# Kernel tuning notes

Hardware: AMD Instinct MI355X
Metric: run time of the kernel (lower is better)

The kernel has to match this reference:

```python
import jax, jax.numpy as jnp
import numpy as np

NUM_HEADS = 8


def setup_inputs() -> dict:
    key = jax.random.key(0)
    ks = jax.random.split(key, 6)
    B, S, H = 2, 4096, 512
    Q = jax.random.normal(ks[0], (B, S, H), dtype=jnp.float32)
    K = jax.random.normal(ks[1], (B, S, H), dtype=jnp.float32)
    V = jax.random.normal(ks[2], (B, S, H), dtype=jnp.float32)
    risk_sigma = jax.random.uniform(ks[3], (B, 1), dtype=jnp.float32) * 0.2
    risk_lambda = jnp.array([2.0], dtype=jnp.float32)
    W_out = jax.random.normal(ks[4], (H, H), dtype=jnp.float32) * (1.0 / np.sqrt(H))
    b_out = jnp.zeros((H,), dtype=jnp.float32)
    return {"Q": Q, "K": K, "V": V, "risk_sigma": risk_sigma,
            "risk_lambda": risk_lambda, "W_out": W_out, "b_out": b_out}


def reference(Q, K, V, risk_sigma, risk_lambda, W_out, b_out):
    B, S, H = Q.shape
    nh = NUM_HEADS
    hd = H // nh
    # split heads: [B, S, nh, hd]
    q = Q.reshape(B, S, nh, hd)
    k = K.reshape(B, S, nh, hd)
    v = V.reshape(B, S, nh, hd)
    scale = 1.0 / jnp.sqrt(jnp.asarray(hd, dtype=Q.dtype))
    # [B, nh, S, S]
    scores = jnp.einsum('bshd,bthd->bhst', q, k) * scale
    # distance-based risk penalty
    pos = jnp.arange(S, dtype=Q.dtype)
    norm_dist = jnp.abs(pos[None, :] - pos[:, None]) / S  # [S, S]
    dist_sq = norm_dist ** 2
    sigma_c = jnp.clip(risk_sigma, 0.001, 0.2)            # [B, 1]
    sigma_n = (sigma_c - 0.001) / (0.2 - 0.001)
    lam = (risk_lambda / 10.0).reshape(())                 # scalar
    risk_term = lam * sigma_n[:, :, None, None] * dist_sq[None, None]  # [B,1,S,S]
    attn = jax.nn.softmax(scores - risk_term, axis=-1)
    ctx = jnp.einsum('bhst,bthd->bshd', attn, v).reshape(B, S, H)
    return ctx @ W_out.T + b_out
```

## Files before the change

### kernel.cpp

```cpp
#include <hip/hip_runtime.h>
#include <hip/hip_bf16.h>


#define S_LEN 4096
#define NHEAD 8
#define HD 64
#define HTOT 512

typedef __attribute__((ext_vector_type(8))) short short8;
typedef __attribute__((ext_vector_type(4))) float floatx4;

#if __has_builtin(__builtin_amdgcn_exp2f)
#define EXP2F(x) __builtin_amdgcn_exp2f(x)
#else
#define EXP2F(x) exp2f(x)
#endif

__device__ __forceinline__ unsigned pack_bf16(float a, float b) {
    unsigned ua = __builtin_bit_cast(unsigned, a) + 0x8000u;
    unsigned ub = __builtin_bit_cast(unsigned, b) + 0x8000u;
    return __builtin_amdgcn_perm(ub, ua, 0x07060302u);
}

__device__ __forceinline__ unsigned short f2bf(float x) {
    unsigned u = __builtin_bit_cast(unsigned, x) + 0x8000u;
    return (unsigned short)(u >> 16);
}

__device__ __forceinline__ void async16(const unsigned short* g, unsigned short* l) {
    __builtin_amdgcn_global_load_lds(
        (const __attribute__((address_space(1))) unsigned int*)g,
        (__attribute__((address_space(3))) unsigned int*)l, 16, 0, 0);
}

__global__ __launch_bounds__(256) void prep_kernel(
    const float* __restrict__ K, unsigned short* __restrict__ K16,
    const float* __restrict__ V, unsigned short* __restrict__ Vt,
    const float* __restrict__ W, unsigned short* __restrict__ W16)
{
    const int tid = threadIdx.x;
    if (blockIdx.x >= 3072) {
        size_t i = ((size_t)(blockIdx.x - 3072) * 256 + tid) * 8;
        float4 a = *(const float4*)(W + i);
        float4 b = *(const float4*)(W + i + 4);
        unsigned o[4] = {pack_bf16(a.x, a.y), pack_bf16(a.z, a.w),
                         pack_bf16(b.x, b.y), pack_bf16(b.z, b.w)};
        *(short8*)(W16 + i) = *(short8*)o;
    } else if (blockIdx.x < 2048) {
        size_t i = ((size_t)blockIdx.x * 256 + tid) * 8;
        float4 a = *(const float4*)(K + i);
        float4 b = *(const float4*)(K + i + 4);
        unsigned o[4] = {pack_bf16(a.x, a.y), pack_bf16(a.z, a.w),
                         pack_bf16(b.x, b.y), pack_bf16(b.z, b.w)};
        *(short8*)(K16 + i) = *(short8*)o;
    } else {
        __shared__ unsigned short T[64 * 66];
        const int blk = blockIdx.x - 2048;
        const int st = blk & 63;
        const int bh = blk >> 6;
        const int b = bh >> 3, h = bh & 7;
        const float* src = V + ((size_t)b * S_LEN + st * 64) * HTOT + h * HD;
        for (int i = 0; i < 4; i++) {
            int idx = tid + i * 256;
            int s = idx >> 4, c4 = idx & 15;
            float4 v = *(const float4*)(src + (size_t)s * HTOT + c4 * 4);
            T[(c4 * 4 + 0) * 66 + s] = f2bf(v.x);
            T[(c4 * 4 + 1) * 66 + s] = f2bf(v.y);
            T[(c4 * 4 + 2) * 66 + s] = f2bf(v.z);
            T[(c4 * 4 + 3) * 66 + s] = f2bf(v.w);
        }
        __syncthreads();
        unsigned short* dst = Vt + ((size_t)bh * 64) * S_LEN + st * 64;
        for (int i = 0; i < 2; i++) {
            int idx = tid + i * 256;
            int d = idx >> 3, c8 = idx & 7;
            uint2 lo = *(const uint2*)&T[d * 66 + c8 * 8];
            uint2 hi = *(const uint2*)&T[d * 66 + c8 * 8 + 4];
            unsigned o[4] = {lo.x, lo.y, hi.x, hi.y};
            *(short8*)(dst + (size_t)d * S_LEN + c8 * 8) = *(short8*)o;
        }
    }
}

__global__ __launch_bounds__(512, 4) void attn_kernel(
    const float* __restrict__ Q, const unsigned short* __restrict__ K16,
    const unsigned short* __restrict__ Vt,
    const float* __restrict__ risk_sigma, const float* __restrict__ risk_lambda,
    unsigned short* __restrict__ ctx)
{
    __shared__ unsigned short SH[32768];

    const int tid  = threadIdx.x;
    const int wave = tid >> 6;
    const int grp  = wave >> 2;
    const int wv   = wave & 3;
    const int lane = tid & 63;
    const int quad = lane >> 4;
    const int ln   = lane & 15;
    const int sw   = ln & 7;

    const int bid = blockIdx.x;
    const int qt  = bid & 31;
    const int h   = (bid >> 5) & 7;
    const int b   = bid >> 8;
    const int qbase = qt * 128;

    float sig = risk_sigma[b];
    sig = fminf(fmaxf(sig, 0.001f), 0.2f);
    const float sn   = (sig - 0.001f) * (1.0f / 0.199f);
    const float coef = risk_lambda[0] * 0.1f * sn;
    const float nc2 = -coef * (1.0f / 4096.0f) * (1.0f / 4096.0f) * 1.4426950408889634f;
    const float qscale = 0.125f * 1.4426950408889634f;

    const float* Qb = Q + (size_t)b * S_LEN * HTOT + (size_t)h * HD;
    const unsigned short* Kb = K16 + (size_t)b * S_LEN * HTOT + (size_t)h * HD;
    const unsigned short* Vb = Vt + ((size_t)(b * 8 + h) * 64) * S_LEN;

    const int rl  = lane >> 3;
    const int c8g = ((lane & 7) ^ rl) << 3;
    const int ksrow = ((wv & 1) << 4) | (((rl >> 2) & 1) << 3)
                    | ((wv >> 1) << 2) | (rl & 3);

    auto dma = [&](int buf, int kb) {
        unsigned short* base = SH + (grp * 2 + buf) * 8192;
        const unsigned short* gk = Kb + (size_t)(kb + ksrow) * HTOT + c8g;
        const unsigned short* gv = Vb + (size_t)(wv * 8 + rl) * S_LEN + kb + c8g;
        async16(gk,              base + wv * 512 + lane * 8);
        async16(gk + 32 * HTOT,  base + (wv + 4) * 512 + lane * 8);
        async16(gv,              base + 4096 + wv * 512 + lane * 8);
        async16(gv + 32 * S_LEN, base + 4096 + (wv + 4) * 512 + lane * 8);
    };

    const int kb0 = grp * 2048;
    dma(0, kb0);

    short8 qf[2][2];
    {
        const float* qp0 = Qb + (size_t)(qbase + wv * 32 + ln) * HTOT + quad * 8;
        #pragma unroll
        for (int nt = 0; nt < 2; nt++) {
            const float* qp = qp0 + (size_t)(nt * 16) * HTOT;
            #pragma unroll
            for (int half = 0; half < 2; half++) {
                float4 x = *(const float4*)(qp + half * 32);
                float4 y = *(const float4*)(qp + half * 32 + 4);
                unsigned o[4] = {pack_bf16(x.x * qscale, x.y * qscale),
                                 pack_bf16(x.z * qscale, x.w * qscale),
                                 pack_bf16(y.x * qscale, y.y * qscale),
                                 pack_bf16(y.z * qscale, y.w * qscale)};
                qf[nt][half] = *(short8*)o;
            }
        }
    }
    __syncthreads();

    const short sone = (short)0x3F80;
    const short8 ones = {sone, sone, sone, sone, sone, sone, sone, sone};

    floatx4 Oacc[2][4], Lacc[2];
    #pragma unroll
    for (int nt = 0; nt < 2; nt++) {
        Lacc[nt] = (floatx4){0.f, 0.f, 0.f, 0.f};
        #pragma unroll
        for (int dt = 0; dt < 4; dt++) Oacc[nt][dt] = (floatx4){0.f, 0.f, 0.f, 0.f};
    }

    const int qa = qbase + wv * 32;
    const float quad8f = (float)(quad * 8);

    for (int kt = 0; kt < 32; ++kt) {
        const int kbase = kb0 + kt * 64;
        const int cur = kt & 1;
        if (kt < 31) dma(1 - cur, kbase + 64);
        const unsigned short* Kc = SH + (grp * 2 + cur) * 8192;
        const unsigned short* Vc = Kc + 4096;

        const float dqq = (float)(qa + ln - kbase) - quad8f;
        unsigned pw[2][2][4];

        #pragma unroll
        for (int jt = 0; jt < 4; jt++) {
            const int krow = (jt * 16 + ln) * 64;
            short8 ak0 = *(const short8*)&Kc[krow + ((quad ^ sw) << 3)];
            short8 ak1 = *(const short8*)&Kc[krow + (((quad + 4) ^ sw) << 3)];
            const float jtoff = (float)((jt >> 1) * 32 + (jt & 1) * 4);
            #pragma unroll
            for (int nt = 0; nt < 2; nt++) {
                float d = dqq + ((float)(nt * 16) - jtoff);
                floatx4 rk;
                #pragma unroll
                for (int r = 0; r < 4; r++) {
                    rk[r] = (nc2 * d) * d;
                    d -= 1.0f;
                }
                floatx4 s = __builtin_amdgcn_mfma_f32_16x16x32_bf16(ak0, qf[nt][0], rk, 0, 0, 0);
                s = __builtin_amdgcn_mfma_f32_16x16x32_bf16(ak1, qf[nt][1], s, 0, 0, 0);
                float p0 = EXP2F(s[0]);
                float p1 = EXP2F(s[1]);
                float p2 = EXP2F(s[2]);
                float p3 = EXP2F(s[3]);
                pw[nt][jt >> 1][(jt & 1) * 2 + 0] = pack_bf16(p0, p1);
                pw[nt][jt >> 1][(jt & 1) * 2 + 1] = pack_bf16(p2, p3);
            }
        }

        __builtin_amdgcn_s_setprio(1);
        #pragma unroll
        for (int dt = 0; dt < 4; dt++) {
            const int vrow = (dt * 16 + ln) * 64;
            short8 bv0 = *(const short8*)&Vc[vrow + ((quad ^ sw) << 3)];
            short8 bv1 = *(const short8*)&Vc[vrow + (((quad + 4) ^ sw) << 3)];
            #pragma unroll
            for (int nt = 0; nt < 2; nt++) {
                short8 pa0 = *(const short8*)&pw[nt][0][0];
                short8 pa1 = *(const short8*)&pw[nt][1][0];
                Oacc[nt][dt] = __builtin_amdgcn_mfma_f32_16x16x32_bf16(pa0, bv0, Oacc[nt][dt], 0, 0, 0);
                Oacc[nt][dt] = __builtin_amdgcn_mfma_f32_16x16x32_bf16(pa1, bv1, Oacc[nt][dt], 0, 0, 0);
            }
        }
        #pragma unroll
        for (int nt = 0; nt < 2; nt++) {
            short8 pa0 = *(const short8*)&pw[nt][0][0];
            short8 pa1 = *(const short8*)&pw[nt][1][0];
            Lacc[nt] = __builtin_amdgcn_mfma_f32_16x16x32_bf16(pa0, ones, Lacc[nt], 0, 0, 0);
            Lacc[nt] = __builtin_amdgcn_mfma_f32_16x16x32_bf16(pa1, ones, Lacc[nt], 0, 0, 0);
        }
        __builtin_amdgcn_s_setprio(0);
        __syncthreads();
    }

    float* X   = (float*)SH;
    float* Lsh = (float*)SH + 128 * 68;

    if (ln == 0) {
        #pragma unroll
        for (int nt = 0; nt < 2; nt++)
            #pragma unroll
            for (int r = 0; r < 4; r++)
                Lsh[grp * 128 + wv * 32 + nt * 16 + quad * 4 + r] = Lacc[nt][r];
    }
    if (grp == 0) {
        #pragma unroll
        for (int nt = 0; nt < 2; nt++)
            #pragma unroll
            for (int dt = 0; dt < 4; dt++)
                #pragma unroll
                for (int r = 0; r < 4; r++)
                    X[(wv * 32 + nt * 16 + quad * 4 + r) * 68 + dt * 16 + ln] = Oacc[nt][dt][r];
    }
    __syncthreads();
    if (grp == 1) {
        #pragma unroll
        for (int nt = 0; nt < 2; nt++) {
            float inv[4];
            #pragma unroll
            for (int r = 0; r < 4; r++) {
                int row = wv * 32 + nt * 16 + quad * 4 + r;
                inv[r] = 1.0f / (Lsh[row] + Lsh[128 + row]);
            }
            #pragma unroll
            for (int dt = 0; dt < 4; dt++)
                #pragma unroll
                for (int r = 0; r < 4; r++) {
                    int row = wv * 32 + nt * 16 + quad * 4 + r;
                    float* p = &X[row * 68 + dt * 16 + ln];
                    *p = (*p + Oacc[nt][dt][r]) * inv[r];
                }
        }
    }
    __syncthreads();
    {
        const int q = tid >> 2;
        const int c = tid & 3;
        const float* xp = X + q * 68 + c * 16;
        float4 x0 = *(const float4*)(xp + 0);
        float4 x1 = *(const float4*)(xp + 4);
        float4 x2 = *(const float4*)(xp + 8);
        float4 x3 = *(const float4*)(xp + 12);
        unsigned o0[4] = {pack_bf16(x0.x, x0.y), pack_bf16(x0.z, x0.w),
                          pack_bf16(x1.x, x1.y), pack_bf16(x1.z, x1.w)};
        unsigned o1[4] = {pack_bf16(x2.x, x2.y), pack_bf16(x2.z, x2.w),
                          pack_bf16(x3.x, x3.y), pack_bf16(x3.z, x3.w)};
        unsigned short* cp = ctx + ((size_t)b * S_LEN + qbase + q) * HTOT + h * HD + c * 16;
        *(short8*)cp       = *(short8*)o0;
        *(short8*)(cp + 8) = *(short8*)o1;
    }
}

__global__ __launch_bounds__(256) void proj_kernel(
    const unsigned short* __restrict__ A,
    const unsigned short* __restrict__ W16,
    const float* __restrict__ bias,
    float* __restrict__ out)
{
    __shared__ unsigned short Ash[2][64 * 32];
    __shared__ unsigned short Bsh[2][128 * 32];
    const int tid = threadIdx.x;
    const int wave = tid >> 6, lane = tid & 63, quad = lane >> 4, ln = lane & 15;
    const int wr = wave >> 1, wc = wave & 1;
    const int m0 = blockIdx.y * 64;
    const int nb = blockIdx.x * 128;

    const int arow = (wave * 64 + lane) >> 2;
    const int ac   = (wave * 64 + lane) & 3;
    const int acs  = (ac ^ ((arow >> 1) & 3)) << 3;
    const int wrow0 = (wave * 64 + lane) >> 2;
    const int wc0   = (wave * 64 + lane) & 3;
    const int wcs0  = (wc0 ^ ((wrow0 >> 1) & 3)) << 3;
    const int wrow1 = wrow0 + 64;
    const int wcs1  = (wc0 ^ ((wrow1 >> 1) & 3)) << 3;

    auto dma = [&](int buf, int k0) {
        async16(A + (size_t)(m0 + arow) * 512 + k0 + acs,
                &Ash[buf][wave * 512 + lane * 8]);
        async16(W16 + (size_t)(nb + wrow0) * 512 + k0 + wcs0,
                &Bsh[buf][wave * 512 + lane * 8]);
        async16(W16 + (size_t)(nb + wrow1) * 512 + k0 + wcs1,
                &Bsh[buf][(wave + 4) * 512 + lane * 8]);
    };

    floatx4 acc[2][4];
    for (int i = 0; i < 2; i++)
        for (int j = 0; j < 4; j++) acc[i][j] = (floatx4){0.f, 0.f, 0.f, 0.f};

    dma(0, 0);
    for (int kt = 0; kt < 16; ++kt) {
        const int cur = kt & 1;
        __syncthreads();
        if (kt < 15) dma(1 - cur, (kt + 1) * 32);

        short8 af[2], bf[4];
        for (int i = 0; i < 2; i++) {
            int r = wr * 32 + i * 16 + ln;
            af[i] = *(const short8*)&Ash[cur][r * 32 + ((quad ^ ((r >> 1) & 3)) << 3)];
        }
        for (int j = 0; j < 4; j++) {
            int r = wc * 64 + j * 16 + ln;
            bf[j] = *(const short8*)&Bsh[cur][r * 32 + ((quad ^ ((r >> 1) & 3)) << 3)];
        }
        for (int i = 0; i < 2; i++)
            for (int j = 0; j < 4; j++)
                acc[i][j] = __builtin_amdgcn_mfma_f32_16x16x32_bf16(af[i], bf[j], acc[i][j], 0, 0, 0);
    }

    for (int i = 0; i < 2; i++) {
        int row = m0 + wr * 32 + i * 16 + quad * 4;
        for (int j = 0; j < 4; j++) {
            int col = nb + wc * 64 + j * 16 + ln;
            float bv = bias[col];
            #pragma unroll
            for (int r = 0; r < 4; r++)
                out[(size_t)(row + r) * 512 + col] = acc[i][j][r] + bv;
        }
    }
}

extern "C" void kernel_launch(void* const* d_in, const int* in_sizes, int n_in,
                              void* d_out, int out_size, void* d_ws, size_t ws_size,
                              hipStream_t stream) {
    const float* Q    = (const float*)d_in[0];
    const float* K    = (const float*)d_in[1];
    const float* V    = (const float*)d_in[2];
    const float* sig  = (const float*)d_in[3];
    const float* lam  = (const float*)d_in[4];
    const float* W    = (const float*)d_in[5];
    const float* bias = (const float*)d_in[6];

    unsigned short* K16 = (unsigned short*)d_ws;
    unsigned short* Vt  = (unsigned short*)((char*)d_ws + (8u << 20));
    unsigned short* ctx = (unsigned short*)((char*)d_ws + (16u << 20));
    unsigned short* W16 = (unsigned short*)((char*)d_ws + (24u << 20));
    float* out = (float*)d_out;

    prep_kernel<<<dim3(3200), dim3(256), 0, stream>>>(K, K16, V, Vt, W, W16);
    attn_kernel<<<dim3(512), dim3(512), 0, stream>>>(Q, K16, Vt, sig, lam, ctx);
    proj_kernel<<<dim3(4, 128), dim3(256), 0, stream>>>(ctx, W16, bias, out);
}
```

Measured before the change: 201.3 us.

## Fuse K/V/W bf16 prep into attention kernel with per-head atomic barrier

Removes the separate prep kernel. Each attention block now converts its slice of K, V (transposed) and W to bf16, then waits on a per-(batch,head) atomic counter barrier across the 32 blocks sharing that head before starting the flash loop. A tiny zero kernel resets the flags. This saves one launch and the gap between kernels, but it relies on all 32 blocks of a head being co-resident, and the spin loop has a guard that could break out early. Probabilities are now packed by truncation instead of rounding, which trims a few ALU ops.

```diff
diff --git a/kernel.cpp b/kernel.cpp
--- a/kernel.cpp
+++ b/kernel.cpp
@@ -3,7 +3,6 @@
 
 
 #define S_LEN 4096
-#define NHEAD 8
 #define HD 64
 #define HTOT 512
 
@@ -22,6 +21,11 @@
     return __builtin_amdgcn_perm(ub, ua, 0x07060302u);
 }
 
+__device__ __forceinline__ unsigned pack_trunc(float a, float b) {
+    return __builtin_amdgcn_perm(__builtin_bit_cast(unsigned, b),
+                                 __builtin_bit_cast(unsigned, a), 0x07060302u);
+}
+
 __device__ __forceinline__ unsigned short f2bf(float x) {
     unsigned u = __builtin_bit_cast(unsigned, x) + 0x8000u;
     return (unsigned short)(u >> 16);
@@ -33,35 +37,70 @@
         (__attribute__((address_space(3))) unsigned int*)l, 16, 0, 0);
 }
 
-__global__ __launch_bounds__(256) void prep_kernel(
-    const float* __restrict__ K, unsigned short* __restrict__ K16,
-    const float* __restrict__ V, unsigned short* __restrict__ Vt,
-    const float* __restrict__ W, unsigned short* __restrict__ W16)
+__device__ __forceinline__ void sync_bh(unsigned* c) {
+    __threadfence();
+    __syncthreads();
+    if (threadIdx.x == 0) {
+        unsigned v = __hip_atomic_fetch_add(c, 1u, __ATOMIC_ACQ_REL,
+                                            __HIP_MEMORY_SCOPE_AGENT);
+        unsigned target = ((v >> 5) + 1u) << 5;
+        int guard = 0;
+        while (__hip_atomic_load(c, __ATOMIC_ACQUIRE,
+                                 __HIP_MEMORY_SCOPE_AGENT) < target) {
+            __builtin_amdgcn_s_sleep(8);
+            if (++guard > (1 << 17)) break;
+        }
+    }
+    __syncthreads();
+    __threadfence();
+}
+
+__global__ void zero_kernel(unsigned* __restrict__ flags) {
+    if (threadIdx.x < 16) flags[threadIdx.x] = 0;
+}
+
+__global__ __launch_bounds__(512, 4) void attn_kernel(
+    const float* __restrict__ Q, const float* __restrict__ K,
+    const float* __restrict__ V, const float* __restrict__ W,
+    const float* __restrict__ risk_sigma, const float* __restrict__ risk_lambda,
+    unsigned short* __restrict__ K16, unsigned short* __restrict__ Vt,
+    unsigned short* __restrict__ W16, unsigned* __restrict__ flags,
+    unsigned short* __restrict__ ctx)
 {
+    __shared__ unsigned short SH[32768];
+
     const int tid = threadIdx.x;
-    if (blockIdx.x >= 3072) {
-        size_t i = ((size_t)(blockIdx.x - 3072) * 256 + tid) * 8;
-        float4 a = *(const float4*)(W + i);
-        float4 b = *(const float4*)(W + i + 4);
-        unsigned o[4] = {pack_bf16(a.x, a.y), pack_bf16(a.z, a.w),
-                         pack_bf16(b.x, b.y), pack_bf16(b.z, b.w)};
-        *(short8*)(W16 + i) = *(short8*)o;
-    } else if (blockIdx.x < 2048) {
-        size_t i = ((size_t)blockIdx.x * 256 + tid) * 8;
-        float4 a = *(const float4*)(K + i);
-        float4 b = *(const float4*)(K + i + 4);
-        unsigned o[4] = {pack_bf16(a.x, a.y), pack_bf16(a.z, a.w),
-                         pack_bf16(b.x, b.y), pack_bf16(b.z, b.w)};
-        *(short8*)(K16 + i) = *(short8*)o;
-    } else {
-        __shared__ unsigned short T[64 * 66];
-        const int blk = blockIdx.x - 2048;
-        const int st = blk & 63;
-        const int bh = blk >> 6;
-        const int b = bh >> 3, h = bh & 7;
+    const int bid = blockIdx.x;
+    const int qt  = bid & 31;
+    const int bh  = bid >> 5;
+    const int b   = bh >> 3;
+    const int h   = bh & 7;
+    const int qbase = qt * 128;
+
+    {
+        const int u   = qt * 512 + tid;
+        const int row = u >> 2;
+        const int c16 = (u & 3) * 16;
+        const size_t off = ((size_t)b * S_LEN + row) * HTOT + h * HD + c16;
+        float4 a0 = *(const float4*)(K + off);
+        float4 a1 = *(const float4*)(K + off + 4);
+        float4 a2 = *(const float4*)(K + off + 8);
+        float4 a3 = *(const float4*)(K + off + 12);
+        unsigned o0[4] = {pack_bf16(a0.x, a0.y), pack_bf16(a0.z, a0.w),
+                          pack_bf16(a1.x, a1.y), pack_bf16(a1.z, a1.w)};
+        unsigned o1[4] = {pack_bf16(a2.x, a2.y), pack_bf16(a2.z, a2.w),
+                          pack_bf16(a3.x, a3.y), pack_bf16(a3.z, a3.w)};
+        *(short8*)(K16 + off)     = *(short8*)o0;
+        *(short8*)(K16 + off + 8) = *(short8*)o1;
+    }
+    {
+        const int vh = tid >> 8;
+        const int t2 = tid & 255;
+        const int st = qt * 2 + vh;
+        unsigned short* T = SH + vh * 4224;
         const float* src = V + ((size_t)b * S_LEN + st * 64) * HTOT + h * HD;
         for (int i = 0; i < 4; i++) {
-            int idx = tid + i * 256;
+            int idx = t2 + i * 256;
             int s = idx >> 4, c4 = idx & 15;
             float4 v = *(const float4*)(src + (size_t)s * HTOT + c4 * 4);
             T[(c4 * 4 + 0) * 66 + s] = f2bf(v.x);
@@ -72,7 +111,7 @@
         __syncthreads();
         unsigned short* dst = Vt + ((size_t)bh * 64) * S_LEN + st * 64;
         for (int i = 0; i < 2; i++) {
-            int idx = tid + i * 256;
+            int idx = t2 + i * 256;
             int d = idx >> 3, c8 = idx & 7;
             uint2 lo = *(const uint2*)&T[d * 66 + c8 * 8];
             uint2 hi = *(const uint2*)&T[d * 66 + c8 * 8 + 4];
@@ -80,210 +119,206 @@
             *(short8*)(dst + (size_t)d * S_LEN + c8 * 8) = *(short8*)o;
         }
     }
-}
-
-__global__ __launch_bounds__(512, 4) void attn_kernel(
-    const float* __restrict__ Q, const unsigned short* __restrict__ K16,
-    const unsigned short* __restrict__ Vt,
-    const float* __restrict__ risk_sigma, const float* __restrict__ risk_lambda,
-    unsigned short* __restrict__ ctx)
-{
-    __shared__ unsigned short SH[32768];
-
-    const int tid  = threadIdx.x;
-    const int wave = tid >> 6;
-    const int grp  = wave >> 2;
-    const int wv   = wave & 3;
-    const int lane = tid & 63;
-    const int quad = lane >> 4;
-    const int ln   = lane & 15;
-    const int sw   = ln & 7;
-
-    const int bid = blockIdx.x;
-    const int qt  = bid & 31;
-    const int h   = (bid >> 5) & 7;
-    const int b   = bid >> 8;
-    const int qbase = qt * 128;
-
-    float sig = risk_sigma[b];
-    sig = fminf(fmaxf(sig, 0.001f), 0.2f);
-    const float sn   = (sig - 0.001f) * (1.0f / 0.199f);
-    const float coef = risk_lambda[0] * 0.1f * sn;
-    const float nc2 = -coef * (1.0f / 4096.0f) * (1.0f / 4096.0f) * 1.4426950408889634f;
-    const float qscale = 0.125f * 1.4426950408889634f;
-
-    const float* Qb = Q + (size_t)b * S_LEN * HTOT + (size_t)h * HD;
-    const unsigned short* Kb = K16 + (size_t)b * S_LEN * HTOT + (size_t)h * HD;
-    const unsigned short* Vb = Vt + ((size_t)(b * 8 + h) * 64) * S_LEN;
-
-    const int rl  = lane >> 3;
-    const int c8g = ((lane & 7) ^ rl) << 3;
-    const int ksrow = ((wv & 1) << 4) | (((rl >> 2) & 1) << 3)
-                    | ((wv >> 1) << 2) | (rl & 3);
-
-    auto dma = [&](int buf, int kb) {
-        unsigned short* base = SH + (grp * 2 + buf) * 8192;
-        const unsigned short* gk = Kb + (size_t)(kb + ksrow) * HTOT + c8g;
-        const unsigned short* gv = Vb + (size_t)(wv * 8 + rl) * S_LEN + kb + c8g;
-        async16(gk,              base + wv * 512 + lane * 8);
-        async16(gk + 32 * HTOT,  base + (wv + 4) * 512 + lane * 8);
-        async16(gv,              base + 4096 + wv * 512 + lane * 8);
-        async16(gv + 32 * S_LEN, base + 4096 + (wv + 4) * 512 + lane * 8);
-    };
-
-    const int kb0 = grp * 2048;
-    dma(0, kb0);
-
-    short8 qf[2][2];
+    if (bid < 64) {
+        size_t i = ((size_t)bid * 512 + tid) * 8;
+        float4 a = *(const float4*)(W + i);
+        float4 c = *(const float4*)(W + i + 4);
+        unsigned o[4] = {pack_bf16(a.x, a.y), pack_bf16(a.z, a.w),
+                         pack_bf16(c.x, c.y), pack_bf16(c.z, c.w)};
+        *(short8*)(W16 + i) = *(short8*)o;
+    }
+
+    sync_bh(&flags[bh]);
+
     {
-        const float* qp0 = Qb + (size_t)(qbase + wv * 32 + ln) * HTOT + quad * 8;
+        const int wave = tid >> 6;
+        const int grp  = wave >> 2;
+        const int wv   = wave & 3;
+        const int lane = tid & 63;
+        const int quad = lane >> 4;
+        const int ln   = lane & 15;
+        const int sw   = ln & 7;
+
+        float sig = risk_sigma[b];
+        sig = fminf(fmaxf(sig, 0.001f), 0.2f);
+        const float sn   = (sig - 0.001f) * (1.0f / 0.199f);
+        const float coef = risk_lambda[0] * 0.1f * sn;
+        const float nc2 = -coef * (1.0f / 4096.0f) * (1.0f / 4096.0f) * 1.4426950408889634f;
+        const float qscale = 0.125f * 1.4426950408889634f;
+
+        const float* Qb = Q + (size_t)b * S_LEN * HTOT + (size_t)h * HD;
+        const unsigned short* Kb = K16 + (size_t)b * S_LEN * HTOT + (size_t)h * HD;
+        const unsigned short* Vb = Vt + ((size_t)(b * 8 + h) * 64) * S_LEN;
+
+        const int rl  = lane >> 3;
+        const int c8g = ((lane & 7) ^ rl) << 3;
+        const int ksrow = ((wv & 1) << 4) | (((rl >> 2) & 1) << 3)
+                        | ((wv >> 1) << 2) | (rl & 3);
+
+        auto dma = [&](int buf, int kb) {
+            unsigned short* base = SH + (grp * 2 + buf) * 8192;
+            const unsigned short* gk = Kb + (size_t)(kb + ksrow) * HTOT + c8g;
+            const unsigned short* gv = Vb + (size_t)(wv * 8 + rl) * S_LEN + kb + c8g;
+            async16(gk,              base + wv * 512 + lane * 8);
+            async16(gk + 32 * HTOT,  base + (wv + 4) * 512 + lane * 8);
+            async16(gv,              base + 4096 + wv * 512 + lane * 8);
+            async16(gv + 32 * S_LEN, base + 4096 + (wv + 4) * 512 + lane * 8);
+        };
+
+        const int kb0 = grp * 2048;
+        dma(0, kb0);
+
+        short8 qf[2][2];
+        {
+            const float* qp0 = Qb + (size_t)(qbase + wv * 32 + ln) * HTOT + quad * 8;
+            #pragma unroll
+            for (int nt = 0; nt < 2; nt++) {
+                const float* qp = qp0 + (size_t)(nt * 16) * HTOT;
+                #pragma unroll
+                for (int hf = 0; hf < 2; hf++) {
+                    float4 x = *(const float4*)(qp + hf * 32);
+                    float4 y = *(const float4*)(qp + hf * 32 + 4);
+                    unsigned o[4] = {pack_bf16(x.x * qscale, x.y * qscale),
+                                     pack_bf16(x.z * qscale, x.w * qscale),
+                                     pack_bf16(y.x * qscale, y.y * qscale),
+                                     pack_bf16(y.z * qscale, y.w * qscale)};
+                    qf[nt][hf] = *(short8*)o;
+                }
+            }
+        }
+        __syncthreads();
+
+        const short sone = (short)0x3F80;
+        const short8 ones = {sone, sone, sone, sone, sone, sone, sone, sone};
+
+        floatx4 Oacc[2][4], Lacc[2];
         #pragma unroll
         for (int nt = 0; nt < 2; nt++) {
-            const float* qp = qp0 + (size_t)(nt * 16) * HTOT;
-            #pragma unroll
-            for (int half = 0; half < 2; half++) {
-                float4 x = *(const float4*)(qp + half * 32);
-                float4 y = *(const float4*)(qp + half * 32 + 4);
-                unsigned o[4] = {pack_bf16(x.x * qscale, x.y * qscale),
-                                 pack_bf16(x.z * qscale, x.w * qscale),
-                                 pack_bf16(y.x * qscale, y.y * qscale),
-                                 pack_bf16(y.z * qscale, y.w * qscale)};
-                qf[nt][half] = *(short8*)o;
+            Lacc[nt] = (floatx4){0.f, 0.f, 0.f, 0.f};
+            #pragma unroll
+            for (int dt = 0; dt < 4; dt++) Oacc[nt][dt] = (floatx4){0.f, 0.f, 0.f, 0.f};
+        }
+
+        const int qa = qbase + wv * 32;
+        const float quad8f = (float)(quad * 8);
+
+        for (int kt = 0; kt < 32; ++kt) {
+            const int kbase = kb0 + kt * 64;
+            const int cur = kt & 1;
+            if (kt < 31) dma(1 - cur, kbase + 64);
+            const unsigned short* Kc = SH + (grp * 2 + cur) * 8192;
+            const unsigned short* Vc = Kc + 4096;
+
+            const float dqq = (float)(qa + ln - kbase) - quad8f;
+            unsigned pw[2][2][4];
+
+            #pragma unroll
+            for (int jt = 0; jt < 4; jt++) {
+                const int krow = (jt * 16 + ln) * 64;
+                short8 ak0 = *(const short8*)&Kc[krow + ((quad ^ sw) << 3)];
+                short8 ak1 = *(const short8*)&Kc[krow + (((quad + 4) ^ sw) << 3)];
+                const float jtoff = (float)((jt >> 1) * 32 + (jt & 1) * 4);
+                #pragma unroll
+                for (int nt = 0; nt < 2; nt++) {
+                    float d = dqq + ((float)(nt * 16) - jtoff);
+                    floatx4 rk;
+                    #pragma unroll
+                    for (int r = 0; r < 4; r++) {
+                        rk[r] = (nc2 * d) * d;
+                        d -= 1.0f;
+                    }
+                    floatx4 s = __builtin_amdgcn_mfma_f32_16x16x32_bf16(ak0, qf[nt][0], rk, 0, 0, 0);
+                    s = __builtin_amdgcn_mfma_f32_16x16x32_bf16(ak1, qf[nt][1], s, 0, 0, 0);
+                    float p0 = EXP2F(s[0]);
+                    float p1 = EXP2F(s[1]);
+                    float p2 = EXP2F(s[2]);
+                    float p3 = EXP2F(s[3]);
+                    pw[nt][jt >> 1][(jt & 1) * 2 + 0] = pack_trunc(p0, p1);
+                    pw[nt][jt >> 1][(jt & 1) * 2 + 1] = pack_trunc(p2, p3);
+                }
             }
-        }
-    }
-    __syncthreads();
-
-    const short sone = (short)0x3F80;
-    const short8 ones = {sone, sone, sone, sone, sone, sone, sone, sone};
-
-    floatx4 Oacc[2][4], Lacc[2];
-    #pragma unroll
-    for (int nt = 0; nt < 2; nt++) {
-        Lacc[nt] = (floatx4){0.f, 0.f, 0.f, 0.f};
-        #pragma unroll
-        for (int dt = 0; dt < 4; dt++) Oacc[nt][dt] = (floatx4){0.f, 0.f, 0.f, 0.f};
-    }
-
-    const int qa = qbase + wv * 32;
-    const float quad8f = (float)(quad * 8);
-
-    for (int kt = 0; kt < 32; ++kt) {
-        const int kbase = kb0 + kt * 64;
-        const int cur = kt & 1;
-        if (kt < 31) dma(1 - cur, kbase + 64);
-        const unsigned short* Kc = SH + (grp * 2 + cur) * 8192;
-        const unsigned short* Vc = Kc + 4096;
-
-        const float dqq = (float)(qa + ln - kbase) - quad8f;
-        unsigned pw[2][2][4];
-
-        #pragma unroll
-        for (int jt = 0; jt < 4; jt++) {
-            const int krow = (jt * 16 + ln) * 64;
-            short8 ak0 = *(const short8*)&Kc[krow + ((quad ^ sw) << 3)];
-            short8 ak1 = *(const short8*)&Kc[krow + (((quad + 4) ^ sw) << 3)];
-            const float jtoff = (float)((jt >> 1) * 32 + (jt & 1) * 4);
-            #pragma unroll
-            for (int nt = 0; nt < 2; nt++) {
-                float d = dqq + ((float)(nt * 16) - jtoff);
-                floatx4 rk;
-                #pragma unroll
-                for (int r = 0; r < 4; r++) {
-                    rk[r] = (nc2 * d) * d;
-                    d -= 1.0f;
+
+            __builtin_amdgcn_s_setprio(1);
+            #pragma unroll
+            for (int dt = 0; dt < 4; dt++) {
+                const int vrow = (dt * 16 + ln) * 64;
+                short8 bv0 = *(const short8*)&Vc[vrow + ((quad ^ sw) << 3)];
+                short8 bv1 = *(const short8*)&Vc[vrow + (((quad + 4) ^ sw) << 3)];
+                #pragma unroll
+                for (int nt = 0; nt < 2; nt++) {
+                    short8 pa0 = *(const short8*)&pw[nt][0][0];
+                    short8 pa1 = *(const short8*)&pw[nt][1][0];
+                    Oacc[nt][dt] = __builtin_amdgcn_mfma_f32_16x16x32_bf16(pa0, bv0, Oacc[nt][dt], 0, 0, 0);
+                    Oacc[nt][dt] = __builtin_amdgcn_mfma_f32_16x16x32_bf16(pa1, bv1, Oacc[nt][dt], 0, 0, 0);
                 }
-                floatx4 s = __builtin_amdgcn_mfma_f32_16x16x32_bf16(ak0, qf[nt][0], rk, 0, 0, 0);
-                s = __builtin_amdgcn_mfma_f32_16x16x32_bf16(ak1, qf[nt][1], s, 0, 0, 0);
-                float p0 = EXP2F(s[0]);
-                float p1 = EXP2F(s[1]);
-                float p2 = EXP2F(s[2]);
-                float p3 = EXP2F(s[3]);
-                pw[nt][jt >> 1][(jt & 1) * 2 + 0] = pack_bf16(p0, p1);
-                pw[nt][jt >> 1][(jt & 1) * 2 + 1] = pack_bf16(p2, p3);
             }
-        }
-
-        __builtin_amdgcn_s_setprio(1);
-        #pragma unroll
-        for (int dt = 0; dt < 4; dt++) {
-            const int vrow = (dt * 16 + ln) * 64;
-            short8 bv0 = *(const short8*)&Vc[vrow + ((quad ^ sw) << 3)];
-            short8 bv1 = *(const short8*)&Vc[vrow + (((quad + 4) ^ sw) << 3)];
             #pragma unroll
             for (int nt = 0; nt < 2; nt++) {
                 short8 pa0 = *(const short8*)&pw[nt][0][0];
                 short8 pa1 = *(const short8*)&pw[nt][1][0];
-                Oacc[nt][dt] = __builtin_amdgcn_mfma_f32_16x16x32_bf16(pa0, bv0, Oacc[nt][dt], 0, 0, 0);
-                Oacc[nt][dt] = __builtin_amdgcn_mfma_f32_16x16x32_bf16(pa1, bv1, Oacc[nt][dt], 0, 0, 0);
+                Lacc[nt] = __builtin_amdgcn_mfma_f32_16x16x32_bf16(pa0, ones, Lacc[nt], 0, 0, 0);
+                Lacc[nt] = __builtin_amdgcn_mfma_f32_16x16x32_bf16(pa1, ones, Lacc[nt], 0, 0, 0);
             }
-        }
-        #pragma unroll
-        for (int nt = 0; nt < 2; nt++) {
-            short8 pa0 = *(const short8*)&pw[nt][0][0];
-            short8 pa1 = *(const short8*)&pw[nt][1][0];
-            Lacc[nt] = __builtin_amdgcn_mfma_f32_16x16x32_bf16(pa0, ones, Lacc[nt], 0, 0, 0);
-            Lacc[nt] = __builtin_amdgcn_mfma_f32_16x16x32_bf16(pa1, ones, Lacc[nt], 0, 0, 0);
-        }
-        __builtin_amdgcn_s_setprio(0);
+            __builtin_amdgcn_s_setprio(0);
+            __syncthreads();
+        }
+
+        float* X   = (float*)SH;
+        float* Lsh = (float*)SH + 128 * 68;
+
+        if (ln == 0) {
+            #pragma unroll
+            for (int nt = 0; nt < 2; nt++)
+                #pragma unroll
+                for (int r = 0; r < 4; r++)
+                    Lsh[grp * 128 + wv * 32 + nt * 16 + quad * 4 + r] = Lacc[nt][r];
+        }
+        if (grp == 0) {
+            #pragma unroll
+            for (int nt = 0; nt < 2; nt++)
+                #pragma unroll
+                for (int dt = 0; dt < 4; dt++)
+                    #pragma unroll
+                    for (int r = 0; r < 4; r++)
+                        X[(wv * 32 + nt * 16 + quad * 4 + r) * 68 + dt * 16 + ln] = Oacc[nt][dt][r];
+        }
         __syncthreads();
-    }
-
-    float* X   = (float*)SH;
-    float* Lsh = (float*)SH + 128 * 68;
-
-    if (ln == 0) {
-        #pragma unroll
-        for (int nt = 0; nt < 2; nt++)
-            #pragma unroll
-            for (int r = 0; r < 4; r++)
-                Lsh[grp * 128 + wv * 32 + nt * 16 + quad * 4 + r] = Lacc[nt][r];
-    }
-    if (grp == 0) {
-        #pragma unroll
-        for (int nt = 0; nt < 2; nt++)
-            #pragma unroll
-            for (int dt = 0; dt < 4; dt++)
-                #pragma unroll
-                for (int r = 0; r < 4; r++)
-                    X[(wv * 32 + nt * 16 + quad * 4 + r) * 68 + dt * 16 + ln] = Oacc[nt][dt][r];
-    }
-    __syncthreads();
-    if (grp == 1) {
-        #pragma unroll
-        for (int nt = 0; nt < 2; nt++) {
-            float inv[4];
-            #pragma unroll
-            for (int r = 0; r < 4; r++) {
-                int row = wv * 32 + nt * 16 + quad * 4 + r;
-                inv[r] = 1.0f / (Lsh[row] + Lsh[128 + row]);
-            }
-            #pragma unroll
-            for (int dt = 0; dt < 4; dt++)
+        if (grp == 1) {
+            #pragma unroll
+            for (int nt = 0; nt < 2; nt++) {
+                float inv[4];
                 #pragma unroll
                 for (int r = 0; r < 4; r++) {
                     int row = wv * 32 + nt * 16 + quad * 4 + r;
-                    float* p = &X[row * 68 + dt * 16 + ln];
-                    *p = (*p + Oacc[nt][dt][r]) * inv[r];
+                    inv[r] = 1.0f / (Lsh[row] + Lsh[128 + row]);
                 }
-        }
-    }
-    __syncthreads();
-    {
-        const int q = tid >> 2;
-        const int c = tid & 3;
-        const float* xp = X + q * 68 + c * 16;
-        float4 x0 = *(const float4*)(xp + 0);
-        float4 x1 = *(const float4*)(xp + 4);
-        float4 x2 = *(const float4*)(xp + 8);
-        float4 x3 = *(const float4*)(xp + 12);
-        unsigned o0[4] = {pack_bf16(x0.x, x0.y), pack_bf16(x0.z, x0.w),
-                          pack_bf16(x1.x, x1.y), pack_bf16(x1.z, x1.w)};
-        unsigned o1[4] = {pack_bf16(x2.x, x2.y), pack_bf16(x2.z, x2.w),
-                          pack_bf16(x3.x, x3.y), pack_bf16(x3.z, x3.w)};
-        unsigned short* cp = ctx + ((size_t)b * S_LEN + qbase + q) * HTOT + h * HD + c * 16;
-        *(short8*)cp       = *(short8*)o0;
-        *(short8*)(cp + 8) = *(short8*)o1;
+                #pragma unroll
+                for (int dt = 0; dt < 4; dt++)
+                    #pragma unroll
+                    for (int r = 0; r < 4; r++) {
+                        int row = wv * 32 + nt * 16 + quad * 4 + r;
+                        float* p = &X[row * 68 + dt * 16 + ln];
+                        *p = (*p + Oacc[nt][dt][r]) * inv[r];
+                    }
+            }
+        }
+        __syncthreads();
+        {
+            const int q = tid >> 2;
+            const int c = tid & 3;
+            const float* xp = X + q * 68 + c * 16;
+            float4 x0 = *(const float4*)(xp + 0);
+            float4 x1 = *(const float4*)(xp + 4);
+            float4 x2 = *(const float4*)(xp + 8);
+            float4 x3 = *(const float4*)(xp + 12);
+            unsigned o0[4] = {pack_bf16(x0.x, x0.y), pack_bf16(x0.z, x0.w),
+                              pack_bf16(x1.x, x1.y), pack_bf16(x1.z, x1.w)};
+            unsigned o1[4] = {pack_bf16(x2.x, x2.y), pack_bf16(x2.z, x2.w),
+                              pack_bf16(x3.x, x3.y), pack_bf16(x3.z, x3.w)};
+            unsigned short* cp = ctx + ((size_t)b * S_LEN + qbase + q) * HTOT + h * HD + c * 16;
+            *(short8*)cp       = *(short8*)o0;
+            *(short8*)(cp + 8) = *(short8*)o1;
+        }
     }
 }
 
@@ -370,9 +405,11 @@
     unsigned short* Vt  = (unsigned short*)((char*)d_ws + (8u << 20));
     unsigned short* ctx = (unsigned short*)((char*)d_ws + (16u << 20));
     unsigned short* W16 = (unsigned short*)((char*)d_ws + (24u << 20));
+    unsigned* flags     = (unsigned*)((char*)d_ws + (24u << 20) + (512u << 10));
     float* out = (float*)d_out;
 
-    prep_kernel<<<dim3(3200), dim3(256), 0, stream>>>(K, K16, V, Vt, W, W16);
-    attn_kernel<<<dim3(512), dim3(512), 0, stream>>>(Q, K16, Vt, sig, lam, ctx);
+    zero_kernel<<<dim3(1), dim3(64), 0, stream>>>(flags);
+    attn_kernel<<<dim3(512), dim3(512), 0, stream>>>(
+        Q, K, V, W, sig, lam, K16, Vt, W16, flags, ctx);
     proj_kernel<<<dim3(4, 128), dim3(256), 0, stream>>>(ctx, W16, bias, out);
 }
```

After: 450.6 us. 124% more time.

## Double attention block to 1024 threads with 16 query rows per wave

Applied to the files above, without the earlier changes.

The attention kernel goes from 512 to 1024 threads per block. Each wave now handles 16 query rows instead of 32, and K and V tile loads are split between wave halves. The risk penalty is computed with incremental FMAs, and P is packed to bf16 by truncation instead of rounding. The aim is more waves to hide latency and fewer VGPRs per wave, at the cost of more K/V LDS reads per query and slightly lower precision for P.

```diff
diff --git a/kernel.cpp b/kernel.cpp
--- a/kernel.cpp
+++ b/kernel.cpp
@@ -3,7 +3,6 @@
 
 
 #define S_LEN 4096
-#define NHEAD 8
 #define HD 64
 #define HTOT 512
 
@@ -20,6 +19,11 @@
     unsigned ua = __builtin_bit_cast(unsigned, a) + 0x8000u;
     unsigned ub = __builtin_bit_cast(unsigned, b) + 0x8000u;
     return __builtin_amdgcn_perm(ub, ua, 0x07060302u);
+}
+
+__device__ __forceinline__ unsigned pack_trunc(float a, float b) {
+    return __builtin_amdgcn_perm(__builtin_bit_cast(unsigned, b),
+                                 __builtin_bit_cast(unsigned, a), 0x07060302u);
 }
 
 __device__ __forceinline__ unsigned short f2bf(float x) {
@@ -82,7 +86,7 @@
     }
 }
 
-__global__ __launch_bounds__(512, 4) void attn_kernel(
+__global__ __launch_bounds__(1024, 8) void attn_kernel(
     const float* __restrict__ Q, const unsigned short* __restrict__ K16,
     const unsigned short* __restrict__ Vt,
     const float* __restrict__ risk_sigma, const float* __restrict__ risk_lambda,
@@ -92,8 +96,8 @@
 
     const int tid  = threadIdx.x;
     const int wave = tid >> 6;
-    const int grp  = wave >> 2;
-    const int wv   = wave & 3;
+    const int grp  = wave >> 3;
+    const int wv   = wave & 7;
     const int lane = tid & 63;
     const int quad = lane >> 4;
     const int ln   = lane & 15;
@@ -110,6 +114,7 @@
     const float sn   = (sig - 0.001f) * (1.0f / 0.199f);
     const float coef = risk_lambda[0] * 0.1f * sn;
     const float nc2 = -coef * (1.0f / 4096.0f) * (1.0f / 4096.0f) * 1.4426950408889634f;
+    const float b1c = nc2, b4c = 4.0f * nc2, b9c = 9.0f * nc2;
     const float qscale = 0.125f * 1.4426950408889634f;
 
     const float* Qb = Q + (size_t)b * S_LEN * HTOT + (size_t)h * HD;
@@ -118,38 +123,38 @@
 
     const int rl  = lane >> 3;
     const int c8g = ((lane & 7) ^ rl) << 3;
-    const int ksrow = ((wv & 1) << 4) | (((rl >> 2) & 1) << 3)
-                    | ((wv >> 1) << 2) | (rl & 3);
+    const int ws  = wv & 3;
+    const int ksrow = ((ws & 1) << 4) | (((rl >> 2) & 1) << 3)
+                    | ((ws >> 1) << 2) | (rl & 3);
 
     auto dma = [&](int buf, int kb) {
         unsigned short* base = SH + (grp * 2 + buf) * 8192;
-        const unsigned short* gk = Kb + (size_t)(kb + ksrow) * HTOT + c8g;
-        const unsigned short* gv = Vb + (size_t)(wv * 8 + rl) * S_LEN + kb + c8g;
-        async16(gk,              base + wv * 512 + lane * 8);
-        async16(gk + 32 * HTOT,  base + (wv + 4) * 512 + lane * 8);
-        async16(gv,              base + 4096 + wv * 512 + lane * 8);
-        async16(gv + 32 * S_LEN, base + 4096 + (wv + 4) * 512 + lane * 8);
+        if (wv < 4) {
+            const unsigned short* gk = Kb + (size_t)(kb + ksrow) * HTOT + c8g;
+            async16(gk,             base + ws * 512 + lane * 8);
+            async16(gk + 32 * HTOT, base + (ws + 4) * 512 + lane * 8);
+        } else {
+            const unsigned short* gv = Vb + (size_t)(ws * 8 + rl) * S_LEN + kb + c8g;
+            async16(gv,              base + 4096 + ws * 512 + lane * 8);
+            async16(gv + 32 * S_LEN, base + 4096 + (ws + 4) * 512 + lane * 8);
+        }
     };
 
     const int kb0 = grp * 2048;
     dma(0, kb0);
 
-    short8 qf[2][2];
+    short8 qf[2];
     {
-        const float* qp0 = Qb + (size_t)(qbase + wv * 32 + ln) * HTOT + quad * 8;
-        #pragma unroll
-        for (int nt = 0; nt < 2; nt++) {
-            const float* qp = qp0 + (size_t)(nt * 16) * HTOT;
-            #pragma unroll
-            for (int half = 0; half < 2; half++) {
-                float4 x = *(const float4*)(qp + half * 32);
-                float4 y = *(const float4*)(qp + half * 32 + 4);
-                unsigned o[4] = {pack_bf16(x.x * qscale, x.y * qscale),
-                                 pack_bf16(x.z * qscale, x.w * qscale),
-                                 pack_bf16(y.x * qscale, y.y * qscale),
-                                 pack_bf16(y.z * qscale, y.w * qscale)};
-                qf[nt][half] = *(short8*)o;
-            }
+        const float* qp = Qb + (size_t)(qbase + wv * 16 + ln) * HTOT + quad * 8;
+        #pragma unroll
+        for (int hf = 0; hf < 2; hf++) {
+            float4 x = *(const float4*)(qp + hf * 32);
+            float4 y = *(const float4*)(qp + hf * 32 + 4);
+            unsigned o[4] = {pack_bf16(x.x * qscale, x.y * qscale),
+                             pack_bf16(x.z * qscale, x.w * qscale),
+                             pack_bf16(y.x * qscale, y.y * qscale),
+                             pack_bf16(y.z * qscale, y.w * qscale)};
+            qf[hf] = *(short8*)o;
         }
     }
     __syncthreads();
@@ -157,15 +162,12 @@
     const short sone = (short)0x3F80;
     const short8 ones = {sone, sone, sone, sone, sone, sone, sone, sone};
 
-    floatx4 Oacc[2][4], Lacc[2];
+    floatx4 Oacc[4], Lacc;
+    Lacc = (floatx4){0.f, 0.f, 0.f, 0.f};
     #pragma unroll
-    for (int nt = 0; nt < 2; nt++) {
-        Lacc[nt] = (floatx4){0.f, 0.f, 0.f, 0.f};
-        #pragma unroll
-        for (int dt = 0; dt < 4; dt++) Oacc[nt][dt] = (floatx4){0.f, 0.f, 0.f, 0.f};
-    }
-
-    const int qa = qbase + wv * 32;
+    for (int dt = 0; dt < 4; dt++) Oacc[dt] = (floatx4){0.f, 0.f, 0.f, 0.f};
+
+    const int qa = qbase + wv * 16;
     const float quad8f = (float)(quad * 8);
 
     for (int kt = 0; kt < 32; ++kt) {
@@ -176,55 +178,44 @@
         const unsigned short* Vc = Kc + 4096;
 
         const float dqq = (float)(qa + ln - kbase) - quad8f;
-        unsigned pw[2][2][4];
+        unsigned pw[2][4];
 
         #pragma unroll
         for (int jt = 0; jt < 4; jt++) {
             const int krow = (jt * 16 + ln) * 64;
             short8 ak0 = *(const short8*)&Kc[krow + ((quad ^ sw) << 3)];
             short8 ak1 = *(const short8*)&Kc[krow + (((quad + 4) ^ sw) << 3)];
-            const float jtoff = (float)((jt >> 1) * 32 + (jt & 1) * 4);
-            #pragma unroll
-            for (int nt = 0; nt < 2; nt++) {
-                float d = dqq + ((float)(nt * 16) - jtoff);
-                floatx4 rk;
-                #pragma unroll
-                for (int r = 0; r < 4; r++) {
-                    rk[r] = (nc2 * d) * d;
-                    d -= 1.0f;
-                }
-                floatx4 s = __builtin_amdgcn_mfma_f32_16x16x32_bf16(ak0, qf[nt][0], rk, 0, 0, 0);
-                s = __builtin_amdgcn_mfma_f32_16x16x32_bf16(ak1, qf[nt][1], s, 0, 0, 0);
-                float p0 = EXP2F(s[0]);
-                float p1 = EXP2F(s[1]);
-                float p2 = EXP2F(s[2]);
-                float p3 = EXP2F(s[3]);
-                pw[nt][jt >> 1][(jt & 1) * 2 + 0] = pack_bf16(p0, p1);
-                pw[nt][jt >> 1][(jt & 1) * 2 + 1] = pack_bf16(p2, p3);
-            }
+            const float d0 = dqq - (float)((jt >> 1) * 32 + (jt & 1) * 4);
+            const float s1 = nc2 * d0;
+            const float t  = s1 * d0;
+            floatx4 rk;
+            rk[0] = t;
+            rk[1] = __builtin_fmaf(-2.0f, s1, t) + b1c;
+            rk[2] = __builtin_fmaf(-4.0f, s1, t) + b4c;
+            rk[3] = __builtin_fmaf(-6.0f, s1, t) + b9c;
+            floatx4 s = __builtin_amdgcn_mfma_f32_16x16x32_bf16(ak0, qf[0], rk, 0, 0, 0);
+            s = __builtin_amdgcn_mfma_f32_16x16x32_bf16(ak1, qf[1], s, 0, 0, 0);
+            float p0 = EXP2F(s[0]);
+            float p1 = EXP2F(s[1]);
+            float p2 = EXP2F(s[2]);
+            float p3 = EXP2F(s[3]);
+            pw[jt >> 1][(jt & 1) * 2 + 0] = pack_trunc(p0, p1);
+            pw[jt >> 1][(jt & 1) * 2 + 1] = pack_trunc(p2, p3);
         }
 
         __builtin_amdgcn_s_setprio(1);
+        short8 pa0 = *(const short8*)&pw[0][0];
+        short8 pa1 = *(const short8*)&pw[1][0];
         #pragma unroll
         for (int dt = 0; dt < 4; dt++) {
             const int vrow = (dt * 16 + ln) * 64;
             short8 bv0 = *(const short8*)&Vc[vrow + ((quad ^ sw) << 3)];
             short8 bv1 = *(const short8*)&Vc[vrow + (((quad + 4) ^ sw) << 3)];
-            #pragma unroll
-            for (int nt = 0; nt < 2; nt++) {
-                short8 pa0 = *(const short8*)&pw[nt][0][0];
-                short8 pa1 = *(const short8*)&pw[nt][1][0];
-                Oacc[nt][dt] = __builtin_amdgcn_mfma_f32_16x16x32_bf16(pa0, bv0, Oacc[nt][dt], 0, 0, 0);
-                Oacc[nt][dt] = __builtin_amdgcn_mfma_f32_16x16x32_bf16(pa1, bv1, Oacc[nt][dt], 0, 0, 0);
-            }
-        }
-        #pragma unroll
-        for (int nt = 0; nt < 2; nt++) {
-            short8 pa0 = *(const short8*)&pw[nt][0][0];
-            short8 pa1 = *(const short8*)&pw[nt][1][0];
-            Lacc[nt] = __builtin_amdgcn_mfma_f32_16x16x32_bf16(pa0, ones, Lacc[nt], 0, 0, 0);
-            Lacc[nt] = __builtin_amdgcn_mfma_f32_16x16x32_bf16(pa1, ones, Lacc[nt], 0, 0, 0);
-        }
+            Oacc[dt] = __builtin_amdgcn_mfma_f32_16x16x32_bf16(pa0, bv0, Oacc[dt], 0, 0, 0);
+            Oacc[dt] = __builtin_amdgcn_mfma_f32_16x16x32_bf16(pa1, bv1, Oacc[dt], 0, 0, 0);
+        }
+        Lacc = __builtin_amdgcn_mfma_f32_16x16x32_bf16(pa0, ones, Lacc, 0, 0, 0);
+        Lacc = __builtin_amdgcn_mfma_f32_16x16x32_bf16(pa1, ones, Lacc, 0, 0, 0);
         __builtin_amdgcn_s_setprio(0);
         __syncthreads();
     }
@@ -234,56 +225,44 @@
 
     if (ln == 0) {
         #pragma unroll
-        for (int nt = 0; nt < 2; nt++)
+        for (int r = 0; r < 4; r++)
+            Lsh[grp * 128 + wv * 16 + quad * 4 + r] = Lacc[r];
+    }
+    if (grp == 0) {
+        #pragma unroll
+        for (int dt = 0; dt < 4; dt++)
             #pragma unroll
             for (int r = 0; r < 4; r++)
-                Lsh[grp * 128 + wv * 32 + nt * 16 + quad * 4 + r] = Lacc[nt][r];
-    }
-    if (grp == 0) {
-        #pragma unroll
-        for (int nt = 0; nt < 2; nt++)
-            #pragma unroll
-            for (int dt = 0; dt < 4; dt++)
-                #pragma unroll
-                for (int r = 0; r < 4; r++)
-                    X[(wv * 32 + nt * 16 + quad * 4 + r) * 68 + dt * 16 + ln] = Oacc[nt][dt][r];
+                X[(wv * 16 + quad * 4 + r) * 68 + dt * 16 + ln] = Oacc[dt][r];
     }
     __syncthreads();
     if (grp == 1) {
-        #pragma unroll
-        for (int nt = 0; nt < 2; nt++) {
-            float inv[4];
+        float inv[4];
+        #pragma unroll
+        for (int r = 0; r < 4; r++) {
+            int row = wv * 16 + quad * 4 + r;
+            inv[r] = 1.0f / (Lsh[row] + Lsh[128 + row]);
+        }
+        #pragma unroll
+        for (int dt = 0; dt < 4; dt++)
             #pragma unroll
             for (int r = 0; r < 4; r++) {
-                int row = wv * 32 + nt * 16 + quad * 4 + r;
-                inv[r] = 1.0f / (Lsh[row] + Lsh[128 + row]);
+                int row = wv * 16 + quad * 4 + r;
+                float* p = &X[row * 68 + dt * 16 + ln];
+                *p = (*p + Oacc[dt][r]) * inv[r];
             }
-            #pragma unroll
-            for (int dt = 0; dt < 4; dt++)
-                #pragma unroll
-                for (int r = 0; r < 4; r++) {
-                    int row = wv * 32 + nt * 16 + quad * 4 + r;
-                    float* p = &X[row * 68 + dt * 16 + ln];
-                    *p = (*p + Oacc[nt][dt][r]) * inv[r];
-                }
-        }
     }
     __syncthreads();
     {
-        const int q = tid >> 2;
-        const int c = tid & 3;
-        const float* xp = X + q * 68 + c * 16;
+        const int q = tid >> 3;
+        const int c = tid & 7;
+        const float* xp = X + q * 68 + c * 8;
         float4 x0 = *(const float4*)(xp + 0);
         float4 x1 = *(const float4*)(xp + 4);
-        float4 x2 = *(const float4*)(xp + 8);
-        float4 x3 = *(const float4*)(xp + 12);
         unsigned o0[4] = {pack_bf16(x0.x, x0.y), pack_bf16(x0.z, x0.w),
                           pack_bf16(x1.x, x1.y), pack_bf16(x1.z, x1.w)};
-        unsigned o1[4] = {pack_bf16(x2.x, x2.y), pack_bf16(x2.z, x2.w),
-                          pack_bf16(x3.x, x3.y), pack_bf16(x3.z, x3.w)};
-        unsigned short* cp = ctx + ((size_t)b * S_LEN + qbase + q) * HTOT + h * HD + c * 16;
-        *(short8*)cp       = *(short8*)o0;
-        *(short8*)(cp + 8) = *(short8*)o1;
+        unsigned short* cp = ctx + ((size_t)b * S_LEN + qbase + q) * HTOT + h * HD + c * 8;
+        *(short8*)cp = *(short8*)o0;
     }
 }
 
@@ -373,6 +352,6 @@
     float* out = (float*)d_out;
 
     prep_kernel<<<dim3(3200), dim3(256), 0, stream>>>(K, K16, V, Vt, W, W16);
-    attn_kernel<<<dim3(512), dim3(512), 0, stream>>>(Q, K16, Vt, sig, lam, ctx);
+    attn_kernel<<<dim3(512), dim3(1024), 0, stream>>>(Q, K16, Vt, sig, lam, ctx);
     proj_kernel<<<dim3(4, 128), dim3(256), 0, stream>>>(ctx, W16, bias, out);
 }
```

Measured after the change: 276.8 us. 1.37x slower.
